# Performance work log

Hardware: AMD Instinct MI355X
Metric: run time of the kernel (lower is better)

The kernel has to match this reference:

```python
import jax, jax.numpy as jnp
import numpy as np

B, C, Q, D = 64, 1024, 256, 128
NEG = -1e30  # VERY_NEGATIVE_NUMBER


def setup_inputs() -> dict:
    key = jax.random.key(0)
    k1, k2, k3, k4, k5, k6 = jax.random.split(key, 6)
    return {
        "x_cont": jax.random.normal(k1, (B, C, D), dtype=jnp.float32),
        "x_ques": jax.random.normal(k2, (B, Q, D), dtype=jnp.float32),
        "c_mask": jnp.ones((B, C), dtype=jnp.float32),
        "q_mask": jnp.ones((B, Q), dtype=jnp.float32),
        "W0": jax.random.uniform(k3, (D, 1), jnp.float32, -0.1, 0.1),
        "W1": jax.random.uniform(k4, (D, 1), jnp.float32, -0.1, 0.1),
        "W2": jax.random.uniform(k5, (1, 1, D), jnp.float32, -0.1, 0.1),
        "bias": jnp.zeros((1,), dtype=jnp.float32),
    }


def reference(x_cont, x_ques, c_mask, q_mask, W0, W1, W2, bias):
    # Trilinear similarity S[b,c,q] = x_cont.W0 + x_ques.W1 + (x_cont*W2).x_ques^T + bias
    s0 = x_cont @ W0                                   # [B,C,1]
    s1 = jnp.swapaxes(x_ques @ W1, 1, 2)               # [B,1,Q]
    s2 = jnp.einsum('bcd,bqd->bcq', x_cont * W2, x_ques)  # [B,C,Q]
    S = s0 + s1 + s2 + bias                            # [B,C,Q]

    qm = q_mask[:, None, :]                            # [B,1,Q]
    cm = c_mask[:, :, None]                            # [B,C,1]
    S_ = jax.nn.softmax(S + NEG * (1.0 - qm), axis=-1)           # row softmax [B,C,Q]
    S_T = jnp.swapaxes(jax.nn.softmax(S + NEG * (1.0 - cm), axis=1), 1, 2)  # [B,Q,C]

    c2q = S_ @ x_ques                                  # [B,C,D]
    q2c = (S_ @ S_T) @ x_cont                          # [B,C,D]
    return jnp.concatenate([x_cont, c2q, x_cont * c2q, x_cont * q2c], axis=-1)
```

## Files before the change

### kernel.cpp

```cpp
#include <hip/hip_runtime.h>
#include <math.h>

#define BB 64
#define CC 1024
#define QQ 256
#define DD 128
#define NEGV (-1.0e30f)

typedef short bf8 __attribute__((ext_vector_type(8)));
typedef short bf4 __attribute__((ext_vector_type(4)));
typedef float f4v __attribute__((ext_vector_type(4)));

__device__ __forceinline__ short f2bf(float f) {
    unsigned u = __builtin_bit_cast(unsigned, f);
    u += 0x7FFFu + ((u >> 16) & 1u);
    return (short)(u >> 16);
}
__device__ __forceinline__ float bf2f(short s) {
    unsigned u = ((unsigned)(unsigned short)s) << 16;
    return __builtin_bit_cast(float, u);
}

__global__ __launch_bounds__(256, 2) void k0_all(
        const float* __restrict__ xc, const float* __restrict__ xq,
        const float* __restrict__ W0, const float* __restrict__ W1,
        const float* __restrict__ W2,
        const float* __restrict__ c_mask, const float* __restrict__ q_mask,
        float* __restrict__ s0m, float* __restrict__ s1m,
        short* __restrict__ xc_bf, short* __restrict__ xqw_bf,
        short* __restrict__ xcT_bf, short* __restrict__ xqT_bf) {
    __shared__ float tile[64][129];
    int bid = blockIdx.x;
    const float *src, *W, *mask;
    float* sm; short *rm, *tr;
    int b, tl, R; bool use2;
    if (bid < 1024) {
        b = ((bid >> 7) << 3) | (bid & 7); tl = (bid >> 3) & 15; R = CC;
        src = xc; W = W0; mask = c_mask; sm = s0m; rm = xc_bf; tr = xcT_bf; use2 = false;
    } else {
        int q = bid - 1024;
        b = ((q >> 5) << 3) | (q & 7); tl = (q >> 3) & 3; R = QQ;
        src = xq; W = W1; mask = q_mask; sm = s1m; rm = xqw_bf; tr = xqT_bf; use2 = true;
    }
    int r0 = tl * 64;
    int t = threadIdx.x;
    int c4 = t & 31, rr = t >> 5;
    float4 wv = ((const float4*)W)[c4];
    float4 sc4 = use2 ? ((const float4*)W2)[c4] : make_float4(1.f, 1.f, 1.f, 1.f);
    const float* sb = src + ((size_t)b * R + r0) * DD;
    #pragma unroll
    for (int p = 0; p < 8; ++p) {
        int row = rr + p * 8;
        float4 g = *(const float4*)&sb[(size_t)row * DD + c4 * 4];
        bf4 o;
        o[0] = f2bf(g.x * sc4.x); o[1] = f2bf(g.y * sc4.y);
        o[2] = f2bf(g.z * sc4.z); o[3] = f2bf(g.w * sc4.w);
        *(bf4*)&rm[((size_t)(b * R + r0 + row)) * DD + c4 * 4] = o;
        float part = g.x * wv.x + g.y * wv.y + g.z * wv.z + g.w * wv.w;
        #pragma unroll
        for (int off = 1; off < 32; off <<= 1) part += __shfl_xor(part, off, 64);
        if ((t & 31) == 0)
            sm[(size_t)b * R + r0 + row] =
                part + NEGV * (1.0f - mask[(size_t)b * R + r0 + row]);
        tile[row][c4 * 4 + 0] = g.x; tile[row][c4 * 4 + 1] = g.y;
        tile[row][c4 * 4 + 2] = g.z; tile[row][c4 * 4 + 3] = g.w;
    }
    __syncthreads();
    int rj = (t & 7) * 8;
    #pragma unroll
    for (int pp = 0; pp < 4; ++pp) {
        int d = pp * 32 + (t >> 3);
        bf8 o;
        #pragma unroll
        for (int j = 0; j < 8; ++j) o[j] = f2bf(tile[rj + j][d]);
        *(bf8*)&tr[((size_t)(b * DD + d)) * R + r0 + rj] = o;
    }
}

#define SCP 1032
#define S2P 264
#define XTP 72

#define K1_LDA(G, S, CT)                                                 \
    {                                                                    \
        const short* ar_ = abase + (size_t)(CT) * 64 * DD;               \
        G[0] = *(const bf8*)&ar_[0];  G[1] = *(const bf8*)&ar_[32];      \
        G[2] = *(const bf8*)&ar_[64]; G[3] = *(const bf8*)&ar_[96];      \
        S = *(const f4v*)&s0base[(CT) * 64];                             \
    }

#define K1_STEPA(G, S, CT)                                                            \
    {                                                                                 \
        f4v acc = {0.f, 0.f, 0.f, 0.f};                                               \
        acc = __builtin_amdgcn_mfma_f32_16x16x32_bf16(G[0], bq[0], acc, 0, 0, 0);     \
        acc = __builtin_amdgcn_mfma_f32_16x16x32_bf16(G[1], bq[1], acc, 0, 0, 0);     \
        acc = __builtin_amdgcn_mfma_f32_16x16x32_bf16(G[2], bq[2], acc, 0, 0, 0);     \
        acc = __builtin_amdgcn_mfma_f32_16x16x32_bf16(G[3], bq[3], acc, 0, 0, 0);     \
        bf4 ov;                                                                       \
        ov[0] = f2bf(acc[0] + S[0]); ov[1] = f2bf(acc[1] + S[1]);                     \
        ov[2] = f2bf(acc[2] + S[2]); ov[3] = f2bf(acc[3] + S[3]);                     \
        *(bf4*)&sc[l16][(CT) * 64 + w * 16 + quad * 4] = ov;                          \
        if ((CT) + 4 < 16) K1_LDA(G, S, (CT) + 4);                                    \
    }

#define K1_LDS2(G, CT)                                                   \
    {                                                                    \
        G[0] = *(const bf8*)&tbase[(CT) * 64];                           \
        G[1] = *(const bf8*)&tbase[(size_t)8 * CC + (CT) * 64];          \
        G[2] = *(const bf8*)&tbase[(size_t)16 * CC + (CT) * 64];         \
        G[3] = *(const bf8*)&tbase[(size_t)24 * CC + (CT) * 64];         \
    }

#define K1_WRS2(G)                                                       \
    {                                                                    \
        *(bf8*)&xct[w][sr][c8l * 8] = G[0];                              \
        *(bf8*)&xct[w][sr + 8][c8l * 8] = G[1];                          \
        *(bf8*)&xct[w][sr + 16][c8l * 8] = G[2];                         \
        *(bf8*)&xct[w][sr + 24][c8l * 8] = G[3];                         \
    }

#define K1_CSTEP(CT)                                                               \
    {                                                                              \
        bf8 a0 = *(const bf8*)&sc[l16][(CT) * 64 + quad * 8];                      \
        bf8 b0 = *(const bf8*)&xct[w][l16][quad * 8];                              \
        acc0 = __builtin_amdgcn_mfma_f32_16x16x32_bf16(a0, b0, acc0, 0, 0, 0);     \
        bf8 b1 = *(const bf8*)&xct[w][16 + l16][quad * 8];                         \
        acc1 = __builtin_amdgcn_mfma_f32_16x16x32_bf16(a0, b1, acc1, 0, 0, 0);     \
        bf8 a1 = *(const bf8*)&sc[l16][(CT) * 64 + 32 + quad * 8];                 \
        bf8 b2 = *(const bf8*)&xct[w][l16][32 + quad * 8];                         \
        acc0 = __builtin_amdgcn_mfma_f32_16x16x32_bf16(a1, b2, acc0, 0, 0, 0);     \
        bf8 b3 = *(const bf8*)&xct[w][16 + l16][32 + quad * 8];                    \
        acc1 = __builtin_amdgcn_mfma_f32_16x16x32_bf16(a1, b3, acc1, 0, 0, 0);     \
    }

__global__ __launch_bounds__(256, 3) void k1_colsm(
        const short* __restrict__ xc_bf, const short* __restrict__ xcT_bf,
        const short* __restrict__ xqw_bf, const float* __restrict__ s0m,
        short* __restrict__ AT) {
    __shared__ __align__(16) short sc[16][SCP];
    __shared__ __align__(16) short xct[4][32][XTP];
    __shared__ float invl[16];

    int bid = blockIdx.x;
    int qt = (bid >> 3) & 15;
    int b = ((bid >> 7) << 3) | (bid & 7);
    int q0 = qt * 16;
    int t = threadIdx.x, w = t >> 6, l = t & 63;
    int quad = l >> 4, l16 = l & 15;

    bf8 bq[4];
    {
        const short* qp = &xqw_bf[(size_t)(b * QQ + q0 + l16) * DD + quad * 8];
        #pragma unroll
        for (int ks = 0; ks < 4; ++ks) bq[ks] = *(const bf8*)&qp[ks * 32];
    }

    const short* abase = &xc_bf[(size_t)(b * CC + w * 16 + l16) * DD + quad * 8];
    const float* s0base = &s0m[b * CC + w * 16 + quad * 4];
    bf8 gA[4], gB[4], gC[4], gD[4];
    f4v sA, sB, sC, sD;
    K1_LDA(gA, sA, 0); K1_LDA(gB, sB, 1); K1_LDA(gC, sC, 2); K1_LDA(gD, sD, 3);
    #pragma unroll
    for (int c4t = 0; c4t < 16; c4t += 4) {
        K1_STEPA(gA, sA, c4t + 0);
        K1_STEPA(gB, sB, c4t + 1);
        K1_STEPA(gC, sC, c4t + 2);
        K1_STEPA(gD, sD, c4t + 3);
    }

    int c8l = l & 7, sr = l >> 3;
    const short* tbase = &xcT_bf[(size_t)(b * DD + w * 32 + sr) * CC + c8l * 8];
    bf8 gS0[4], gS1[4];
    K1_LDS2(gS0, 0);
    K1_LDS2(gS1, 1);

    __syncthreads();

    {
        int q = t >> 4, k = t & 15;
        bf8 v[8];
        #pragma unroll
        for (int j = 0; j < 8; ++j) v[j] = *(const bf8*)&sc[q][k * 8 + j * 128];
        float m = -3.0e38f;
        #pragma unroll
        for (int j = 0; j < 8; ++j)
            #pragma unroll
            for (int e = 0; e < 8; ++e) m = fmaxf(m, bf2f(v[j][e]));
        #pragma unroll
        for (int off = 1; off < 16; off <<= 1) m = fmaxf(m, __shfl_xor(m, off, 64));
        float sum = 0.f;
        #pragma unroll
        for (int j = 0; j < 8; ++j) {
            bf8 o;
            #pragma unroll
            for (int e = 0; e < 8; ++e) {
                float ex = __expf(bf2f(v[j][e]) - m);
                sum += ex;
                o[e] = f2bf(ex);
            }
            *(bf8*)&sc[q][k * 8 + j * 128] = o;
        }
        #pragma unroll
        for (int off = 1; off < 16; off <<= 1) sum += __shfl_xor(sum, off, 64);
        if (k == 0) invl[q] = 1.0f / sum;
    }
    __syncthreads();

    f4v acc0 = {0.f, 0.f, 0.f, 0.f}, acc1 = {0.f, 0.f, 0.f, 0.f};
    K1_WRS2(gS0);
    K1_LDS2(gS0, 2);
    #pragma unroll
    for (int ct = 0; ct < 16; ++ct) {
        K1_CSTEP(ct);
        if (ct < 15) {
            if ((ct & 1) == 0) {
                K1_WRS2(gS1);
                if (ct + 3 < 16) K1_LDS2(gS1, ct + 3);
            } else {
                K1_WRS2(gS0);
                if (ct + 3 < 16) K1_LDS2(gS0, ct + 3);
            }
        }
    }
    {
        bf4 o0, o1;
        #pragma unroll
        for (int r = 0; r < 4; ++r) {
            float il = invl[quad * 4 + r];
            o0[r] = f2bf(acc0[r] * il);
            o1[r] = f2bf(acc1[r] * il);
        }
        int d0 = w * 32 + l16;
        *(bf4*)&AT[(size_t)(b * DD + d0) * QQ + q0 + quad * 4] = o0;
        *(bf4*)&AT[(size_t)(b * DD + d0 + 16) * QQ + q0 + quad * 4] = o1;
    }
}

#define K2_LDA(G, CT)                                                    \
    {                                                                    \
        const short* ar_ = abase + (size_t)(CT) * 64 * DD;               \
        G[0] = *(const bf8*)&ar_[0];  G[1] = *(const bf8*)&ar_[32];      \
        G[2] = *(const bf8*)&ar_[64]; G[3] = *(const bf8*)&ar_[96];      \
    }

#define K2_STEP1(G, SV, QT)                                                           \
    {                                                                                 \
        f4v acc0 = {0.f, 0.f, 0.f, 0.f}, acc1 = {0.f, 0.f, 0.f, 0.f};                 \
        acc0 = __builtin_amdgcn_mfma_f32_16x16x32_bf16(G[0], bc0[0], acc0, 0, 0, 0);  \
        acc1 = __builtin_amdgcn_mfma_f32_16x16x32_bf16(G[0], bc1[0], acc1, 0, 0, 0);  \
        acc0 = __builtin_amdgcn_mfma_f32_16x16x32_bf16(G[1], bc0[1], acc0, 0, 0, 0);  \
        acc1 = __builtin_amdgcn_mfma_f32_16x16x32_bf16(G[1], bc1[1], acc1, 0, 0, 0);  \
        acc0 = __builtin_amdgcn_mfma_f32_16x16x32_bf16(G[2], bc0[2], acc0, 0, 0, 0);  \
        acc1 = __builtin_amdgcn_mfma_f32_16x16x32_bf16(G[2], bc1[2], acc1, 0, 0, 0);  \
        acc0 = __builtin_amdgcn_mfma_f32_16x16x32_bf16(G[3], bc0[3], acc0, 0, 0, 0);  \
        acc1 = __builtin_amdgcn_mfma_f32_16x16x32_bf16(G[3], bc1[3], acc1, 0, 0, 0);  \
        int qbase_ = (QT) * 64 + w * 16 + quad * 4;                                   \
        bf4 o0, o1;                                                                   \
        o0[0] = f2bf(acc0[0] + SV[0]); o0[1] = f2bf(acc0[1] + SV[1]);                 \
        o0[2] = f2bf(acc0[2] + SV[2]); o0[3] = f2bf(acc0[3] + SV[3]);                 \
        o1[0] = f2bf(acc1[0] + SV[0]); o1[1] = f2bf(acc1[1] + SV[1]);                 \
        o1[2] = f2bf(acc1[2] + SV[2]); o1[3] = f2bf(acc1[3] + SV[3]);                 \
        *(bf4*)&sc2[l16][qbase_] = o0;                                                \
        *(bf4*)&sc2[16 + l16][qbase_] = o1;                                           \
    }

#define K2_SRC(NT) ((NT) < 4 ? (qtb + (size_t)((NT) & 3) * 64) : (atb + (size_t)((NT) - 4) * 64))

#define K2_LDS2(G, NT)                                                   \
    {                                                                    \
        const short* gs_ = K2_SRC(NT);                                   \
        G[0] = *(const bf8*)&gs_[0];                                     \
        G[1] = *(const bf8*)&gs_[(size_t)8 * QQ];                        \
        G[2] = *(const bf8*)&gs_[(size_t)16 * QQ];                       \
        G[3] = *(const bf8*)&gs_[(size_t)24 * QQ];                       \
    }

#define K2_WRS2(G)                                                       \
    {                                                                    \
        *(bf8*)&tT[w][sr][c8l * 8] = G[0];                               \
        *(bf8*)&tT[w][sr + 8][c8l * 8] = G[1];                           \
        *(bf8*)&tT[w][sr + 16][c8l * 8] = G[2];                          \
        *(bf8*)&tT[w][sr + 24][c8l * 8] = G[3];                          \
    }

#define K2_CSTEP(TL)                                                                   \
    {                                                                                  \
        int qoff_ = ((TL) & 3) * 64;                                                   \
        _Pragma("unroll")                                                              \
        for (int ks = 0; ks < 2; ++ks) {                                               \
            bf8 a0 = *(const bf8*)&sc2[l16][qoff_ + ks * 32 + quad * 8];               \
            bf8 a1 = *(const bf8*)&sc2[16 + l16][qoff_ + ks * 32 + quad * 8];          \
            bf8 b0 = *(const bf8*)&tT[w][l16][ks * 32 + quad * 8];                     \
            bf8 b1 = *(const bf8*)&tT[w][16 + l16][ks * 32 + quad * 8];                \
            if ((TL) < 4) {                                                            \
                ac[0][0] = __builtin_amdgcn_mfma_f32_16x16x32_bf16(a0, b0, ac[0][0], 0, 0, 0); \
                ac[0][1] = __builtin_amdgcn_mfma_f32_16x16x32_bf16(a0, b1, ac[0][1], 0, 0, 0); \
                ac[1][0] = __builtin_amdgcn_mfma_f32_16x16x32_bf16(a1, b0, ac[1][0], 0, 0, 0); \
                ac[1][1] = __builtin_amdgcn_mfma_f32_16x16x32_bf16(a1, b1, ac[1][1], 0, 0, 0); \
            } else {                                                                   \
                aq[0][0] = __builtin_amdgcn_mfma_f32_16x16x32_bf16(a0, b0, aq[0][0], 0, 0, 0); \
                aq[0][1] = __builtin_amdgcn_mfma_f32_16x16x32_bf16(a0, b1, aq[0][1], 0, 0, 0); \
                aq[1][0] = __builtin_amdgcn_mfma_f32_16x16x32_bf16(a1, b0, aq[1][0], 0, 0, 0); \
                aq[1][1] = __builtin_amdgcn_mfma_f32_16x16x32_bf16(a1, b1, aq[1][1], 0, 0, 0); \
            }                                                                          \
        }                                                                              \
    }

__global__ __launch_bounds__(256, 4) void k2_rowsm(
        const float* __restrict__ xc, const short* __restrict__ xc_bf,
        const short* __restrict__ xqw_bf, const short* __restrict__ xqT_bf,
        const short* __restrict__ AT, const float* __restrict__ s1m,
        float* __restrict__ out) {
    __shared__ __align__(16) short sc2[32][S2P];
    __shared__ __align__(16) short tT[4][32][XTP];
    __shared__ float invl2[32];

    int bid = blockIdx.x;
    int cb = (bid >> 3) & 31;
    int b = ((bid >> 8) << 3) | (bid & 7);
    int c0g = cb * 32;
    int t = threadIdx.x, w = t >> 6, l = t & 63;
    int quad = l >> 4, l16 = l & 15;

    bf8 bc0[4], bc1[4];
    {
        const short* p0 = &xc_bf[(size_t)(b * CC + c0g + l16) * DD + quad * 8];
        const short* p1 = p0 + 16 * DD;
        #pragma unroll
        for (int ks = 0; ks < 4; ++ks) {
            bc0[ks] = *(const bf8*)&p0[ks * 32];
            bc1[ks] = *(const bf8*)&p1[ks * 32];
        }
    }

    const short* abase = &xqw_bf[(size_t)(b * QQ + w * 16 + l16) * DD + quad * 8];
    const float* s1base = &s1m[b * QQ + w * 16 + quad * 4];
    f4v sv0 = *(const f4v*)&s1base[0];
    f4v sv1 = *(const f4v*)&s1base[64];
    f4v sv2 = *(const f4v*)&s1base[128];
    f4v sv3 = *(const f4v*)&s1base[192];
    bf8 gA[4], gB[4];
    K2_LDA(gA, 0); K2_LDA(gB, 1);
    K2_STEP1(gA, sv0, 0); K2_LDA(gA, 2);
    K2_STEP1(gB, sv1, 1); K2_LDA(gB, 3);
    K2_STEP1(gA, sv2, 2);
    K2_STEP1(gB, sv3, 3);

    int c8l = l & 7, sr = l >> 3;
    const short* qtb = &xqT_bf[(size_t)(b * DD + w * 32 + sr) * QQ + c8l * 8];
    const short* atb = &AT[(size_t)(b * DD + w * 32 + sr) * QQ + c8l * 8];
    bf8 gS0[4], gS1[4];
    K2_LDS2(gS0, 0);
    K2_LDS2(gS1, 1);

    __syncthreads();

    {
        int c = t >> 3, k = t & 7;
        bf8 v[4];
        #pragma unroll
        for (int j = 0; j < 4; ++j) v[j] = *(const bf8*)&sc2[c][k * 8 + j * 64];
        float m = -3.0e38f;
        #pragma unroll
        for (int j = 0; j < 4; ++j)
            #pragma unroll
            for (int e = 0; e < 8; ++e) m = fmaxf(m, bf2f(v[j][e]));
        #pragma unroll
        for (int off = 1; off < 8; off <<= 1) m = fmaxf(m, __shfl_xor(m, off, 64));
        float sum = 0.f;
        #pragma unroll
        for (int j = 0; j < 4; ++j) {
            bf8 o;
            #pragma unroll
            for (int e = 0; e < 8; ++e) {
                float ex = __expf(bf2f(v[j][e]) - m);
                sum += ex;
                o[e] = f2bf(ex);
            }
            *(bf8*)&sc2[c][k * 8 + j * 64] = o;
        }
        #pragma unroll
        for (int off = 1; off < 8; off <<= 1) sum += __shfl_xor(sum, off, 64);
        if (k == 0) invl2[c] = 1.0f / sum;
    }
    __syncthreads();

    f4v ac[2][2], aq[2][2];
    f4v zz = {0.f, 0.f, 0.f, 0.f};
    #pragma unroll
    for (int i = 0; i < 2; ++i)
        #pragma unroll
        for (int j = 0; j < 2; ++j) { ac[i][j] = zz; aq[i][j] = zz; }
    K2_WRS2(gS0);
    K2_LDS2(gS0, 2);
    #pragma unroll
    for (int tl = 0; tl < 8; ++tl) {
        K2_CSTEP(tl);
        if (tl < 7) {
            if ((tl & 1) == 0) {
                K2_WRS2(gS1);
                if (tl + 3 < 8) K2_LDS2(gS1, tl + 3);
            } else {
                K2_WRS2(gS0);
                if (tl + 3 < 8) K2_LDS2(gS0, tl + 3);
            }
        }
    }

    __syncthreads();
    float (*c2l)[132] = (float(*)[132])sc2;
    float (*q2l)[132] = (float(*)[132])tT;
    #pragma unroll
    for (int cf = 0; cf < 2; ++cf)
        #pragma unroll
        for (int df = 0; df < 2; ++df)
            #pragma unroll
            for (int r = 0; r < 4; ++r) {
                int cl = cf * 16 + quad * 4 + r;
                int d = w * 32 + df * 16 + l16;
                c2l[cl][d] = ac[cf][df][r];
                q2l[cl][d] = aq[cf][df][r];
            }
    __syncthreads();
    {
        int cl = t >> 3, j4 = (t & 7) * 4;
        float il = invl2[cl];
        const float* xrow = xc + (size_t)(b * CC + c0g + cl) * DD;
        float* orow = out + (size_t)(b * CC + c0g + cl) * (4 * DD);
        #pragma unroll
        for (int ps = 0; ps < 4; ++ps) {
            int d = ps * 32 + j4;
            float4 xv = *(const float4*)&xrow[d];
            float4 cv = *(const float4*)&c2l[cl][d];
            float4 qv = *(const float4*)&q2l[cl][d];
            cv.x *= il; cv.y *= il; cv.z *= il; cv.w *= il;
            qv.x *= il; qv.y *= il; qv.z *= il; qv.w *= il;
            *(float4*)&orow[d] = xv;
            *(float4*)&orow[DD + d] = cv;
            float4 m2 = make_float4(xv.x * cv.x, xv.y * cv.y, xv.z * cv.z, xv.w * cv.w);
            *(float4*)&orow[2 * DD + d] = m2;
            float4 m3 = make_float4(xv.x * qv.x, xv.y * qv.y, xv.z * qv.z, xv.w * qv.w);
            *(float4*)&orow[3 * DD + d] = m3;
        }
    }
}

extern "C" void kernel_launch(void* const* d_in, const int* in_sizes, int n_in,
                              void* d_out, int out_size, void* d_ws, size_t ws_size,
                              hipStream_t stream) {
    const float* x_cont = (const float*)d_in[0];
    const float* x_ques = (const float*)d_in[1];
    const float* c_mask = (const float*)d_in[2];
    const float* q_mask = (const float*)d_in[3];
    const float* W0     = (const float*)d_in[4];
    const float* W1     = (const float*)d_in[5];
    const float* W2     = (const float*)d_in[6];
    float* out = (float*)d_out;

    char* ws = (char*)d_ws;
    float* s0m    = (float*)ws;  ws += (size_t)BB * CC * 4;
    float* s1m    = (float*)ws;  ws += (size_t)BB * QQ * 4;
    short* xc_bf  = (short*)ws;  ws += (size_t)BB * CC * DD * 2;
    short* xqw_bf = (short*)ws;  ws += (size_t)BB * QQ * DD * 2;
    short* xcT_bf = (short*)ws;  ws += (size_t)BB * CC * DD * 2;
    short* xqT_bf = (short*)ws;  ws += (size_t)BB * QQ * DD * 2;
    short* AT     = (short*)ws;

    k0_all<<<BB * 16 + BB * 4, 256, 0, stream>>>(x_cont, x_ques, W0, W1, W2,
                                                 c_mask, q_mask, s0m, s1m,
                                                 xc_bf, xqw_bf, xcT_bf, xqT_bf);
    k1_colsm<<<BB * 16, 256, 0, stream>>>(xc_bf, xcT_bf, xqw_bf, s0m, AT);
    k2_rowsm<<<BB * 32, 256, 0, stream>>>(x_cont, xc_bf, xqw_bf, xqT_bf, AT, s1m, out);
}
```

Before: 258.4 us.

## Compute similarity GEMM once into fp32 buffer shared by both softmax kernels

Adds a dedicated GEMM kernel that computes the bilinear similarity term once per batch and stores it as fp32 in a [B,Q,C] workspace. Both the column-softmax and row-softmax kernels then read this buffer instead of each recomputing the GEMM with MFMA. This removes the duplicated matrix multiply but adds a 64 MB fp32 write plus two full reads, and one extra kernel launch. The occupancy hint on k0 is also raised.

```diff
diff --git a/kernel.cpp b/kernel.cpp
--- a/kernel.cpp
+++ b/kernel.cpp
@@ -21,7 +21,7 @@
     return __builtin_bit_cast(float, u);
 }
 
-__global__ __launch_bounds__(256, 2) void k0_all(
+__global__ __launch_bounds__(256, 4) void k0_all(
         const float* __restrict__ xc, const float* __restrict__ xq,
         const float* __restrict__ W0, const float* __restrict__ W1,
         const float* __restrict__ W2,
@@ -77,31 +77,56 @@
     }
 }
 
+__global__ __launch_bounds__(256, 4) void kS_gemm(
+        const short* __restrict__ xc_bf, const short* __restrict__ xqw_bf,
+        float* __restrict__ S0T) {
+    int bid = blockIdx.x;
+    int idx = (bid >> 3) & 31;
+    int b = ((bid >> 8) << 3) | (bid & 7);
+    int qt = idx >> 3, ct = idx & 7;
+    int t = threadIdx.x, w = t >> 6, l = t & 63;
+    int quad = l >> 4, l16 = l & 15;
+
+    const short* ab = &xqw_bf[(size_t)(b * QQ + qt * 64 + w * 16 + l16) * DD + quad * 8];
+    bf8 a0 = *(const bf8*)&ab[0];
+    bf8 a1 = *(const bf8*)&ab[32];
+    bf8 a2 = *(const bf8*)&ab[64];
+    bf8 a3 = *(const bf8*)&ab[96];
+
+    const short* bbase = &xc_bf[(size_t)(b * CC + ct * 128 + l16) * DD + quad * 8];
+    bf8 bb[2][4];
+    #pragma unroll
+    for (int ks = 0; ks < 4; ++ks) bb[0][ks] = *(const bf8*)&bbase[ks * 32];
+
+    f4v acc[8];
+    #pragma unroll
+    for (int nf = 0; nf < 8; ++nf) acc[nf] = (f4v){0.f, 0.f, 0.f, 0.f};
+
+    #pragma unroll
+    for (int nf = 0; nf < 8; ++nf) {
+        if (nf < 7) {
+            const short* nb = bbase + (size_t)(nf + 1) * 16 * DD;
+            #pragma unroll
+            for (int ks = 0; ks < 4; ++ks) bb[(nf + 1) & 1][ks] = *(const bf8*)&nb[ks * 32];
+        }
+        const bf8* c = bb[nf & 1];
+        acc[nf] = __builtin_amdgcn_mfma_f32_16x16x32_bf16(a0, c[0], acc[nf], 0, 0, 0);
+        acc[nf] = __builtin_amdgcn_mfma_f32_16x16x32_bf16(a1, c[1], acc[nf], 0, 0, 0);
+        acc[nf] = __builtin_amdgcn_mfma_f32_16x16x32_bf16(a2, c[2], acc[nf], 0, 0, 0);
+        acc[nf] = __builtin_amdgcn_mfma_f32_16x16x32_bf16(a3, c[3], acc[nf], 0, 0, 0);
+    }
+
+    size_t obase = (size_t)(b * QQ + qt * 64 + w * 16 + quad * 4) * CC + ct * 128 + l16;
+    #pragma unroll
+    for (int r = 0; r < 4; ++r)
+        #pragma unroll
+        for (int nf = 0; nf < 8; ++nf)
+            S0T[obase + (size_t)r * CC + nf * 16] = acc[r < 4 ? nf : nf][r];
+}
+
 #define SCP 1032
 #define S2P 264
 #define XTP 72
-
-#define K1_LDA(G, S, CT)                                                 \
-    {                                                                    \
-        const short* ar_ = abase + (size_t)(CT) * 64 * DD;               \
-        G[0] = *(const bf8*)&ar_[0];  G[1] = *(const bf8*)&ar_[32];      \
-        G[2] = *(const bf8*)&ar_[64]; G[3] = *(const bf8*)&ar_[96];      \
-        S = *(const f4v*)&s0base[(CT) * 64];                             \
-    }
-
-#define K1_STEPA(G, S, CT)                                                            \
-    {                                                                                 \
-        f4v acc = {0.f, 0.f, 0.f, 0.f};                                               \
-        acc = __builtin_amdgcn_mfma_f32_16x16x32_bf16(G[0], bq[0], acc, 0, 0, 0);     \
-        acc = __builtin_amdgcn_mfma_f32_16x16x32_bf16(G[1], bq[1], acc, 0, 0, 0);     \
-        acc = __builtin_amdgcn_mfma_f32_16x16x32_bf16(G[2], bq[2], acc, 0, 0, 0);     \
-        acc = __builtin_amdgcn_mfma_f32_16x16x32_bf16(G[3], bq[3], acc, 0, 0, 0);     \
-        bf4 ov;                                                                       \
-        ov[0] = f2bf(acc[0] + S[0]); ov[1] = f2bf(acc[1] + S[1]);                     \
-        ov[2] = f2bf(acc[2] + S[2]); ov[3] = f2bf(acc[3] + S[3]);                     \
-        *(bf4*)&sc[l16][(CT) * 64 + w * 16 + quad * 4] = ov;                          \
-        if ((CT) + 4 < 16) K1_LDA(G, S, (CT) + 4);                                    \
-    }
 
 #define K1_LDS2(G, CT)                                                   \
     {                                                                    \
@@ -134,9 +159,8 @@
     }
 
 __global__ __launch_bounds__(256, 3) void k1_colsm(
-        const short* __restrict__ xc_bf, const short* __restrict__ xcT_bf,
-        const short* __restrict__ xqw_bf, const float* __restrict__ s0m,
-        short* __restrict__ AT) {
+        const float* __restrict__ S0T, const short* __restrict__ xcT_bf,
+        const float* __restrict__ s0m, short* __restrict__ AT) {
     __shared__ __align__(16) short sc[16][SCP];
     __shared__ __align__(16) short xct[4][32][XTP];
     __shared__ float invl[16];
@@ -148,24 +172,21 @@
     int t = threadIdx.x, w = t >> 6, l = t & 63;
     int quad = l >> 4, l16 = l & 15;
 
-    bf8 bq[4];
-    {
-        const short* qp = &xqw_bf[(size_t)(b * QQ + q0 + l16) * DD + quad * 8];
-        #pragma unroll
-        for (int ks = 0; ks < 4; ++ks) bq[ks] = *(const bf8*)&qp[ks * 32];
-    }
-
-    const short* abase = &xc_bf[(size_t)(b * CC + w * 16 + l16) * DD + quad * 8];
-    const float* s0base = &s0m[b * CC + w * 16 + quad * 4];
-    bf8 gA[4], gB[4], gC[4], gD[4];
-    f4v sA, sB, sC, sD;
-    K1_LDA(gA, sA, 0); K1_LDA(gB, sB, 1); K1_LDA(gC, sC, 2); K1_LDA(gD, sD, 3);
-    #pragma unroll
-    for (int c4t = 0; c4t < 16; c4t += 4) {
-        K1_STEPA(gA, sA, c4t + 0);
-        K1_STEPA(gB, sB, c4t + 1);
-        K1_STEPA(gC, sC, c4t + 2);
-        K1_STEPA(gD, sD, c4t + 3);
+    {
+        int fq = t & 15, fseg = t >> 4;
+        const float4* srow = (const float4*)(S0T + (size_t)(b * QQ + q0 + fq) * CC + fseg * 64);
+        const float4* brow = (const float4*)(s0m + (size_t)b * CC + fseg * 64);
+        #pragma unroll
+        for (int j = 0; j < 8; ++j) {
+            float4 v0 = srow[2 * j], v1 = srow[2 * j + 1];
+            float4 m0 = brow[2 * j], m1 = brow[2 * j + 1];
+            bf8 o;
+            o[0] = f2bf(v0.x + m0.x); o[1] = f2bf(v0.y + m0.y);
+            o[2] = f2bf(v0.z + m0.z); o[3] = f2bf(v0.w + m0.w);
+            o[4] = f2bf(v1.x + m1.x); o[5] = f2bf(v1.y + m1.y);
+            o[6] = f2bf(v1.z + m1.z); o[7] = f2bf(v1.w + m1.w);
+            *(bf8*)&sc[fq][fseg * 64 + j * 8] = o;
+        }
     }
 
     int c8l = l & 7, sr = l >> 3;
@@ -235,34 +256,6 @@
         *(bf4*)&AT[(size_t)(b * DD + d0 + 16) * QQ + q0 + quad * 4] = o1;
     }
 }
-
-#define K2_LDA(G, CT)                                                    \
-    {                                                                    \
-        const short* ar_ = abase + (size_t)(CT) * 64 * DD;               \
-        G[0] = *(const bf8*)&ar_[0];  G[1] = *(const bf8*)&ar_[32];      \
-        G[2] = *(const bf8*)&ar_[64]; G[3] = *(const bf8*)&ar_[96];      \
-    }
-
-#define K2_STEP1(G, SV, QT)                                                           \
-    {                                                                                 \
-        f4v acc0 = {0.f, 0.f, 0.f, 0.f}, acc1 = {0.f, 0.f, 0.f, 0.f};                 \
-        acc0 = __builtin_amdgcn_mfma_f32_16x16x32_bf16(G[0], bc0[0], acc0, 0, 0, 0);  \
-        acc1 = __builtin_amdgcn_mfma_f32_16x16x32_bf16(G[0], bc1[0], acc1, 0, 0, 0);  \
-        acc0 = __builtin_amdgcn_mfma_f32_16x16x32_bf16(G[1], bc0[1], acc0, 0, 0, 0);  \
-        acc1 = __builtin_amdgcn_mfma_f32_16x16x32_bf16(G[1], bc1[1], acc1, 0, 0, 0);  \
-        acc0 = __builtin_amdgcn_mfma_f32_16x16x32_bf16(G[2], bc0[2], acc0, 0, 0, 0);  \
-        acc1 = __builtin_amdgcn_mfma_f32_16x16x32_bf16(G[2], bc1[2], acc1, 0, 0, 0);  \
-        acc0 = __builtin_amdgcn_mfma_f32_16x16x32_bf16(G[3], bc0[3], acc0, 0, 0, 0);  \
-        acc1 = __builtin_amdgcn_mfma_f32_16x16x32_bf16(G[3], bc1[3], acc1, 0, 0, 0);  \
-        int qbase_ = (QT) * 64 + w * 16 + quad * 4;                                   \
-        bf4 o0, o1;                                                                   \
-        o0[0] = f2bf(acc0[0] + SV[0]); o0[1] = f2bf(acc0[1] + SV[1]);                 \
-        o0[2] = f2bf(acc0[2] + SV[2]); o0[3] = f2bf(acc0[3] + SV[3]);                 \
-        o1[0] = f2bf(acc1[0] + SV[0]); o1[1] = f2bf(acc1[1] + SV[1]);                 \
-        o1[2] = f2bf(acc1[2] + SV[2]); o1[3] = f2bf(acc1[3] + SV[3]);                 \
-        *(bf4*)&sc2[l16][qbase_] = o0;                                                \
-        *(bf4*)&sc2[16 + l16][qbase_] = o1;                                           \
-    }
 
 #define K2_SRC(NT) ((NT) < 4 ? (qtb + (size_t)((NT) & 3) * 64) : (atb + (size_t)((NT) - 4) * 64))
 
@@ -307,10 +300,9 @@
     }
 
 __global__ __launch_bounds__(256, 4) void k2_rowsm(
-        const float* __restrict__ xc, const short* __restrict__ xc_bf,
-        const short* __restrict__ xqw_bf, const short* __restrict__ xqT_bf,
-        const short* __restrict__ AT, const float* __restrict__ s1m,
-        float* __restrict__ out) {
+        const float* __restrict__ xc, const float* __restrict__ S0T,
+        const short* __restrict__ xqT_bf, const short* __restrict__ AT,
+        const float* __restrict__ s1m, float* __restrict__ out) {
     __shared__ __align__(16) short sc2[32][S2P];
     __shared__ __align__(16) short tT[4][32][XTP];
     __shared__ float invl2[32];
@@ -322,29 +314,18 @@
     int t = threadIdx.x, w = t >> 6, l = t & 63;
     int quad = l >> 4, l16 = l & 15;
 
-    bf8 bc0[4], bc1[4];
-    {
-        const short* p0 = &xc_bf[(size_t)(b * CC + c0g + l16) * DD + quad * 8];
-        const short* p1 = p0 + 16 * DD;
-        #pragma unroll
-        for (int ks = 0; ks < 4; ++ks) {
-            bc0[ks] = *(const bf8*)&p0[ks * 32];
-            bc1[ks] = *(const bf8*)&p1[ks * 32];
-        }
-    }
-
-    const short* abase = &xqw_bf[(size_t)(b * QQ + w * 16 + l16) * DD + quad * 8];
-    const float* s1base = &s1m[b * QQ + w * 16 + quad * 4];
-    f4v sv0 = *(const f4v*)&s1base[0];
-    f4v sv1 = *(const f4v*)&s1base[64];
-    f4v sv2 = *(const f4v*)&s1base[128];
-    f4v sv3 = *(const f4v*)&s1base[192];
-    bf8 gA[4], gB[4];
-    K2_LDA(gA, 0); K2_LDA(gB, 1);
-    K2_STEP1(gA, sv0, 0); K2_LDA(gA, 2);
-    K2_STEP1(gB, sv1, 1); K2_LDA(gB, 3);
-    K2_STEP1(gA, sv2, 2);
-    K2_STEP1(gB, sv3, 3);
+    {
+        const float4* srow = (const float4*)(S0T + (size_t)(b * QQ + t) * CC + c0g);
+        float s1v = s1m[(size_t)b * QQ + t];
+        #pragma unroll
+        for (int j = 0; j < 8; ++j) {
+            float4 v = srow[j];
+            sc2[j * 4 + 0][t] = f2bf(v.x + s1v);
+            sc2[j * 4 + 1][t] = f2bf(v.y + s1v);
+            sc2[j * 4 + 2][t] = f2bf(v.z + s1v);
+            sc2[j * 4 + 3][t] = f2bf(v.w + s1v);
+        }
+    }
 
     int c8l = l & 7, sr = l >> 3;
     const short* qtb = &xqT_bf[(size_t)(b * DD + w * 32 + sr) * QQ + c8l * 8];
@@ -464,11 +445,13 @@
     short* xqw_bf = (short*)ws;  ws += (size_t)BB * QQ * DD * 2;
     short* xcT_bf = (short*)ws;  ws += (size_t)BB * CC * DD * 2;
     short* xqT_bf = (short*)ws;  ws += (size_t)BB * QQ * DD * 2;
-    short* AT     = (short*)ws;
+    short* AT     = (short*)ws;  ws += (size_t)BB * DD * QQ * 2;
+    float* S0T    = (float*)ws;
 
     k0_all<<<BB * 16 + BB * 4, 256, 0, stream>>>(x_cont, x_ques, W0, W1, W2,
                                                  c_mask, q_mask, s0m, s1m,
                                                  xc_bf, xqw_bf, xcT_bf, xqT_bf);
-    k1_colsm<<<BB * 16, 256, 0, stream>>>(xc_bf, xcT_bf, xqw_bf, s0m, AT);
-    k2_rowsm<<<BB * 32, 256, 0, stream>>>(x_cont, xc_bf, xqw_bf, xqT_bf, AT, s1m, out);
-}
+    kS_gemm<<<BB * 32, 256, 0, stream>>>(xc_bf, xqw_bf, S0T);
+    k1_colsm<<<BB * 16, 256, 0, stream>>>(S0T, xcT_bf, s0m, AT);
+    k2_rowsm<<<BB * 32, 256, 0, stream>>>(x_cont, S0T, xqT_bf, AT, s1m, out);
+}
```

After: 272.4 us. +5.4%, slower.
